# Performance work log

Hardware: AMD Instinct MI355X
Metric: run time of the kernel (lower is better)

## Reference

```python
import jax, jax.numpy as jnp
import numpy as np
from jax import lax

PATCH = 4
EMBED = 96


def setup_inputs() -> dict:
    key = jax.random.key(0)
    k1, k2, k3, k4, k5 = jax.random.split(key, 5)
    rgb = jax.random.normal(k1, (8, 3, 512, 512), dtype=jnp.float32)
    hs = jax.random.normal(k2, (8, 4, 512, 512), dtype=jnp.float32)
    dem = jax.random.normal(k3, (8, 1, 512, 512), dtype=jnp.float32)
    W = jax.random.normal(k4, (EMBED, 1, PATCH, PATCH), dtype=jnp.float32) * 0.05
    b = jax.random.normal(k5, (EMBED,), dtype=jnp.float32) * 0.05
    return {"rgb": rgb, "hs": hs, "dem": dem, "W": W, "b": b}


def reference(rgb, hs, dem, W, b):
    # Concatenate modalities along channel dim: [B, C=8, H, Wd]
    x = jnp.concatenate([rgb, hs, dem], axis=1)
    B, C, H, Wd = x.shape
    # Pad H, W up to a multiple of patch size (right/bottom), as in _padding
    pad_h = (-H) % PATCH
    pad_w = (-Wd) % PATCH
    if pad_h or pad_w:
        x = jnp.pad(x, ((0, 0), (0, 0), (0, pad_h), (0, pad_w)))
    H2, W2 = x.shape[2], x.shape[3]
    # Each channel goes through the SAME 1->embed_dim conv; fold channels into batch
    xc = x.reshape(B * C, 1, H2, W2)
    y = lax.conv_general_dilated(
        xc, W,
        window_strides=(PATCH, PATCH),
        padding='VALID',
        dimension_numbers=('NCHW', 'OIHW', 'NCHW'),
    ) + b[None, :, None, None]
    Hp, Wp = y.shape[2], y.shape[3]
    # Unfold back and concat per-channel embeddings along channel dim: [B, C*embed, Hp, Wp]
    y = y.reshape(B, C * EMBED, Hp, Wp)
    return y
```

## Files before the change

### kernel.cpp

```cpp
#include <hip/hip_runtime.h>
#include <hip/hip_bf16.h>

#define PATCH 4
#define EMBED 96
#define HIN 512
#define WIN 512
#define HP 128
#define WP 128
#define BATCH 8
#define CHAN 8

__global__ __launch_bounds__(256, 4)
void patch_embed_kernel(const float* __restrict__ rgb,
                        const float* __restrict__ hs,
                        const float* __restrict__ dem,
                        const float* __restrict__ W,
                        const float* __restrict__ bias,
                        float* __restrict__ out) {
    const int blk = blockIdx.x;
    const int hp2 = blk & 63;
    const int bc  = blk >> 6;
    const int b   = bc >> 3;
    const int c   = bc & 7;

    const int tid = threadIdx.x;
    const int hp  = hp2 * 2 + (tid >> 7);
    const int wp  = tid & 127;

    const float* src;
    if (c < 3)      src = rgb + (size_t)(b * 3 + c)       * (HIN * WIN);
    else if (c < 7) src = hs  + (size_t)(b * 4 + (c - 3)) * (HIN * WIN);
    else            src = dem + (size_t)b                 * (HIN * WIN);

    const float* row0 = src + (size_t)(hp * PATCH) * WIN + wp * PATCH;
    const float4 p0 = *(const float4*)(row0);
    const float4 p1 = *(const float4*)(row0 + WIN);
    const float4 p2 = *(const float4*)(row0 + 2 * WIN);
    const float4 p3 = *(const float4*)(row0 + 3 * WIN);

    float* outp = out + (((size_t)(b * CHAN * EMBED + c * EMBED) * HP + hp) * WP + wp);

    #pragma unroll 4
    for (int e = 0; e < EMBED; ++e) {
        const float4 w0 = *(const float4*)(W + e * 16);
        const float4 w1 = *(const float4*)(W + e * 16 + 4);
        const float4 w2 = *(const float4*)(W + e * 16 + 8);
        const float4 w3 = *(const float4*)(W + e * 16 + 12);
        float acc = bias[e];
        acc = fmaf(p0.x, w0.x, acc); acc = fmaf(p0.y, w0.y, acc);
        acc = fmaf(p0.z, w0.z, acc); acc = fmaf(p0.w, w0.w, acc);
        acc = fmaf(p1.x, w1.x, acc); acc = fmaf(p1.y, w1.y, acc);
        acc = fmaf(p1.z, w1.z, acc); acc = fmaf(p1.w, w1.w, acc);
        acc = fmaf(p2.x, w2.x, acc); acc = fmaf(p2.y, w2.y, acc);
        acc = fmaf(p2.z, w2.z, acc); acc = fmaf(p2.w, w2.w, acc);
        acc = fmaf(p3.x, w3.x, acc); acc = fmaf(p3.y, w3.y, acc);
        acc = fmaf(p3.z, w3.z, acc); acc = fmaf(p3.w, w3.w, acc);
        outp[(size_t)e * (HP * WP)] = acc;
    }
}

extern "C" void kernel_launch(void* const* d_in, const int* in_sizes, int n_in,
                              void* d_out, int out_size, void* d_ws, size_t ws_size,
                              hipStream_t stream) {
    const float* rgb  = (const float*)d_in[0];
    const float* hs   = (const float*)d_in[1];
    const float* dem  = (const float*)d_in[2];
    const float* W    = (const float*)d_in[3];
    const float* bias = (const float*)d_in[4];
    float* out = (float*)d_out;

    const int grid = BATCH * CHAN * (HP / 2);
    patch_embed_kernel<<<grid, 256, 0, stream>>>(rgb, hs, dem, W, bias, out);
}
```

Measured before the change: 469.9 us.

## Compute four patches per thread with shared-memory weights and float4 stores

Each thread now computes four adjacent output patches and writes them with one float4 store per embedding channel, instead of one scalar store. Weights and bias are staged once per block in shared memory rather than reloaded from global memory by every thread. The grid shrinks fourfold and launch bounds drop to 2 blocks per CU. This trades occupancy and register pressure for wider stores and weight reuse in a kernel dominated by output writes.

```diff
diff --git a/kernel.cpp b/kernel.cpp
--- a/kernel.cpp
+++ b/kernel.cpp
@@ -10,52 +10,67 @@
 #define BATCH 8
 #define CHAN 8
 
-__global__ __launch_bounds__(256, 4)
+__device__ __forceinline__ float dot4(float4 a, float4 b, float acc) {
+    acc = fmaf(a.x, b.x, acc);
+    acc = fmaf(a.y, b.y, acc);
+    acc = fmaf(a.z, b.z, acc);
+    acc = fmaf(a.w, b.w, acc);
+    return acc;
+}
+
+__global__ __launch_bounds__(256, 2)
 void patch_embed_kernel(const float* __restrict__ rgb,
                         const float* __restrict__ hs,
                         const float* __restrict__ dem,
                         const float* __restrict__ W,
                         const float* __restrict__ bias,
                         float* __restrict__ out) {
+    __shared__ float sW[EMBED * 16 + EMBED];
+
+    const int tid = threadIdx.x;
+    for (int i = tid; i < EMBED * 16 + EMBED; i += 256) {
+        sW[i] = (i < EMBED * 16) ? W[i] : bias[i - EMBED * 16];
+    }
+
     const int blk = blockIdx.x;
-    const int hp2 = blk & 63;
-    const int bc  = blk >> 6;
+    const int hq  = blk & 15;
+    const int bc  = blk >> 4;
     const int b   = bc >> 3;
     const int c   = bc & 7;
 
-    const int tid = threadIdx.x;
-    const int hp  = hp2 * 2 + (tid >> 7);
-    const int wp  = tid & 127;
+    const int hp  = hq * 8 + (tid >> 5);
+    const int wp0 = (tid & 31) * 4;
 
     const float* src;
     if (c < 3)      src = rgb + (size_t)(b * 3 + c)       * (HIN * WIN);
     else if (c < 7) src = hs  + (size_t)(b * 4 + (c - 3)) * (HIN * WIN);
     else            src = dem + (size_t)b                 * (HIN * WIN);
 
-    const float* row0 = src + (size_t)(hp * PATCH) * WIN + wp * PATCH;
-    const float4 p0 = *(const float4*)(row0);
-    const float4 p1 = *(const float4*)(row0 + WIN);
-    const float4 p2 = *(const float4*)(row0 + 2 * WIN);
-    const float4 p3 = *(const float4*)(row0 + 3 * WIN);
+    const float* p = src + (size_t)(hp * PATCH) * WIN + wp0 * PATCH;
+    float4 r[4][4];
+    #pragma unroll
+    for (int dy = 0; dy < 4; ++dy) {
+        #pragma unroll
+        for (int k = 0; k < 4; ++k) {
+            r[dy][k] = *(const float4*)(p + dy * WIN + k * 4);
+        }
+    }
 
-    float* outp = out + (((size_t)(b * CHAN * EMBED + c * EMBED) * HP + hp) * WP + wp);
+    __syncthreads();
 
-    #pragma unroll 4
+    float* outp = out + (((size_t)(b * CHAN * EMBED + c * EMBED)) * HP + hp) * WP + wp0;
+
+    #pragma unroll 2
     for (int e = 0; e < EMBED; ++e) {
-        const float4 w0 = *(const float4*)(W + e * 16);
-        const float4 w1 = *(const float4*)(W + e * 16 + 4);
-        const float4 w2 = *(const float4*)(W + e * 16 + 8);
-        const float4 w3 = *(const float4*)(W + e * 16 + 12);
-        float acc = bias[e];
-        acc = fmaf(p0.x, w0.x, acc); acc = fmaf(p0.y, w0.y, acc);
-        acc = fmaf(p0.z, w0.z, acc); acc = fmaf(p0.w, w0.w, acc);
-        acc = fmaf(p1.x, w1.x, acc); acc = fmaf(p1.y, w1.y, acc);
-        acc = fmaf(p1.z, w1.z, acc); acc = fmaf(p1.w, w1.w, acc);
-        acc = fmaf(p2.x, w2.x, acc); acc = fmaf(p2.y, w2.y, acc);
-        acc = fmaf(p2.z, w2.z, acc); acc = fmaf(p2.w, w2.w, acc);
-        acc = fmaf(p3.x, w3.x, acc); acc = fmaf(p3.y, w3.y, acc);
-        acc = fmaf(p3.z, w3.z, acc); acc = fmaf(p3.w, w3.w, acc);
-        outp[(size_t)e * (HP * WP)] = acc;
+        const float4* wr = (const float4*)(sW + e * 16);
+        const float4 w0 = wr[0], w1 = wr[1], w2 = wr[2], w3 = wr[3];
+        const float bb = sW[EMBED * 16 + e];
+        float4 o;
+        o.x = dot4(r[3][0], w3, dot4(r[2][0], w2, dot4(r[1][0], w1, dot4(r[0][0], w0, bb))));
+        o.y = dot4(r[3][1], w3, dot4(r[2][1], w2, dot4(r[1][1], w1, dot4(r[0][1], w0, bb))));
+        o.z = dot4(r[3][2], w3, dot4(r[2][2], w2, dot4(r[1][2], w1, dot4(r[0][2], w0, bb))));
+        o.w = dot4(r[3][3], w3, dot4(r[2][3], w2, dot4(r[1][3], w1, dot4(r[0][3], w0, bb))));
+        *(float4*)(outp + (size_t)e * (HP * WP)) = o;
     }
 }
 
@@ -69,6 +84,6 @@
     const float* bias = (const float*)d_in[4];
     float* out = (float*)d_out;
 
-    const int grid = BATCH * CHAN * (HP / 2);
+    const int grid = BATCH * CHAN * (HP / 8);
     patch_embed_kernel<<<grid, 256, 0, stream>>>(rgb, hs, dem, W, bias, out);
 }
```

After: 498.4 us. 6.1% more time.
